# Kernel optimization log

Measured on AMD Instinct MI355X. Metric: run time of the kernel, lower is better.

## Reference

```python
import jax, jax.numpy as jnp
import numpy as np
import math

OUT = 7   # output_size
SR = 2    # sampling_ratio


def _roi_align(feat, rois5, scale):
    """torchvision roi_align (aligned=False) for all rois against one FPN level.
    feat: [B,C,H,W], rois5: [N,5] = (batch_idx, x1, y1, x2, y2). Returns [N,C,OUT,OUT]."""
    B, C, H, W = feat.shape
    b = rois5[:, 0].astype(jnp.int32)
    x1 = rois5[:, 1] * scale
    y1 = rois5[:, 2] * scale
    x2 = rois5[:, 3] * scale
    y2 = rois5[:, 4] * scale
    rw = jnp.maximum(x2 - x1, 1.0)
    rh = jnp.maximum(y2 - y1, 1.0)
    gh = OUT * SR  # sampling grid: ph*SR+iy, sample at (g+0.5)*bin/SR from roi start
    gw = OUT * SR
    ys = y1[:, None] + (jnp.arange(gh, dtype=feat.dtype) + 0.5)[None, :] * (rh / gh)[:, None]  # [N,gh]
    xs = x1[:, None] + (jnp.arange(gw, dtype=feat.dtype) + 0.5)[None, :] * (rw / gw)[:, None]  # [N,gw]
    # torchvision bilinear_interpolate: out-of-range (< -1 or > size) -> 0, else clamp
    vy = (ys >= -1.0) & (ys <= H)
    vx = (xs >= -1.0) & (xs <= W)
    y = jnp.clip(ys, 0.0, H - 1)
    x = jnp.clip(xs, 0.0, W - 1)
    y0f = jnp.floor(y)
    x0f = jnp.floor(x)
    y0 = y0f.astype(jnp.int32)
    x0 = x0f.astype(jnp.int32)
    y1i = jnp.minimum(y0 + 1, H - 1)
    x1i = jnp.minimum(x0 + 1, W - 1)
    ly = y - y0f; hy = 1.0 - ly
    lx = x - x0f; hx = 1.0 - lx
    fT = jnp.transpose(feat, (0, 2, 3, 1))  # [B,H,W,C]

    def gather(yi, xi):
        return fT[b[:, None, None], yi[:, :, None], xi[:, None, :]]  # [N,gh,gw,C]

    w00 = (hy[:, :, None] * hx[:, None, :])[..., None]
    w01 = (hy[:, :, None] * lx[:, None, :])[..., None]
    w10 = (ly[:, :, None] * hx[:, None, :])[..., None]
    w11 = (ly[:, :, None] * lx[:, None, :])[..., None]
    val = (gather(y0, x0) * w00 + gather(y0, x1i) * w01
           + gather(y1i, x0) * w10 + gather(y1i, x1i) * w11)
    val = val * (vy[:, :, None] & vx[:, None, :])[..., None].astype(feat.dtype)
    # average SRxSR samples per output bin -> [N,OUT,OUT,C] -> [N,C,OUT,OUT]
    val = val.reshape(val.shape[0], OUT, SR, OUT, SR, C).mean(axis=(2, 4))
    return jnp.transpose(val, (0, 3, 1, 2))


def setup_inputs() -> dict:
    key = jax.random.key(0)
    ks = jax.random.split(key, 6)
    feat0 = jax.random.normal(ks[0], (2, 256, 200, 200), jnp.float32)
    feat1 = jax.random.normal(ks[1], (2, 256, 100, 100), jnp.float32)
    feat2 = jax.random.normal(ks[2], (2, 256, 50, 50), jnp.float32)
    feat3 = jax.random.normal(ks[3], (2, 256, 25, 25), jnp.float32)
    B, N = 2, 512
    xy1 = jax.random.uniform(ks[4], (B, N, 2), jnp.float32, 0.0, 700.0)
    wh = jax.random.uniform(ks[5], (B, N, 2), jnp.float32, 16.0, 320.0)
    xy2 = jnp.minimum(xy1 + wh, 799.0)
    rois = jnp.concatenate([xy1, xy2], axis=-1)  # [B,N,4] = (x1,y1,x2,y2)
    return {"feat0": feat0, "feat1": feat1, "feat2": feat2, "feat3": feat3,
            "rois": rois, "image_h": 800, "image_w": 800}


def reference(feat0, feat1, feat2, feat3, rois, image_h, image_w):
    feats = [feat0, feat1, feat2, feat3]
    B, N = rois.shape[:2]
    # _convert_to_roi_format: prepend batch index column
    bcol = jnp.repeat(jnp.arange(B, dtype=rois.dtype), N)[:, None]
    rois5 = jnp.concatenate([bcol, rois.reshape(-1, 4)], axis=1)  # [B*N,5]
    # _setup_scales / _get_scales: pow-2-rounded ratio of feature H to image H (static)
    scales = [2.0 ** round(math.log2(f.shape[2] / float(image_h))) for f in feats]
    lvl_min = -math.log2(scales[0])   # 2
    lvl_max = -math.log2(scales[-1])  # 5
    # FPN level routing: k = floor(4 + log2(sqrt(area)/224)), clamped
    area = (rois5[:, 4] - rois5[:, 2]) * (rois5[:, 3] - rois5[:, 1])
    k = jnp.floor(4.0 + jnp.log2(jnp.sqrt(area) / 224.0))
    k = jnp.clip(k, lvl_min, lvl_max) - lvl_min  # in {0,1,2,3}
    out = jnp.zeros((B * N, feats[0].shape[1], OUT, OUT), feats[0].dtype)
    for lvl, (f, s) in enumerate(zip(feats, scales)):
        pooled = _roi_align(f, rois5, s)
        out = jnp.where((k == lvl)[:, None, None, None], pooled, out)
    return out
```

## Files before the change

kernel.cpp:

```cpp
#include <hip/hip_runtime.h>

#define OUTS 7
#define SR 2
#define GRIDW 14
#define NS 196
#define NCH 256
#define NROI 1024
#define NBIN 49

#define L0_OFF 0
#define L1_OFF 20480000
#define L2_OFF 25600000
#define L3_OFF 26880000
#define WS_ELEMS 27200000


static __device__ __forceinline__ unsigned short f2bf(float f) {
    unsigned u = __builtin_bit_cast(unsigned, f);
    u += 0x7fffu + ((u >> 16) & 1u);
    return (unsigned short)(u >> 16);
}

__global__ __launch_bounds__(256) void nchw_to_nhwc_bf16(
    const float* __restrict__ f0, const float* __restrict__ f1,
    const float* __restrict__ f2, const float* __restrict__ f3,
    unsigned short* __restrict__ ws) {
    __shared__ float tile[64][65];
    int bid = blockIdx.x;
    const float* in; unsigned short* outp; int P, ptiles, local;
    if (bid < 5000)      { in = f0; outp = ws + L0_OFF; P = 40000; ptiles = 625; local = bid; }
    else if (bid < 6256) { in = f1; outp = ws + L1_OFF; P = 10000; ptiles = 157; local = bid - 5000; }
    else if (bid < 6576) { in = f2; outp = ws + L2_OFF; P = 2500;  ptiles = 40;  local = bid - 6256; }
    else                 { in = f3; outp = ws + L3_OFF; P = 625;   ptiles = 10;  local = bid - 6576; }
    int pt = local % ptiles;
    int rest = local / ptiles;
    int c0 = (rest & 3) * 64;
    int b  = rest >> 2;
    int p0 = pt * 64;
    int tx = threadIdx.x;
    int ty = threadIdx.y;
    const float* inb = in + (size_t)b * NCH * P;
    unsigned short* outb = outp + (size_t)b * P * NCH;

    int p = p0 + tx;
    if (p < P) {
#pragma unroll
        for (int i = 0; i < 16; ++i) {
            int cl = ty * 16 + i;
            tile[cl][tx] = inb[(size_t)(c0 + cl) * P + p];
        }
    }
    __syncthreads();
#pragma unroll
    for (int i = 0; i < 8; ++i) {
        int pl = ty * 16 + i * 2 + (tx >> 5);
        int cl = (tx & 31) * 2;
        int pp = p0 + pl;
        if (pp < P) {
            unsigned lo = f2bf(tile[cl][pl]);
            unsigned hi = f2bf(tile[cl + 1][pl]);
            *(unsigned*)(outb + (size_t)pp * NCH + c0 + cl) = lo | (hi << 16);
        }
    }
}

__global__ __launch_bounds__(256) void roi_gather_nhwc(
    const unsigned short* __restrict__ nhwc,
    const float* __restrict__ rois,
    float* __restrict__ out) {
    __shared__ int   s_off[4][NS];
    __shared__ float s_w[4][NS];
    __shared__ float lds_out[25 * 260];

    int n = blockIdx.x;
    int tid = threadIdx.x;
    int b = n >> 9;

    float x1 = rois[n * 4 + 0];
    float y1 = rois[n * 4 + 1];
    float x2 = rois[n * 4 + 2];
    float y2 = rois[n * 4 + 3];
    float area = (y2 - y1) * (x2 - x1);
    float kf = floorf(4.0f + log2f(sqrtf(area) / 224.0f));
    kf = fminf(fmaxf(kf, 2.0f), 5.0f);
    int lvl = (int)kf - 2;
    float scale = ldexpf(0.25f, -lvl);
    int H, W; size_t base;
    switch (lvl) {
        case 0:  H = 200; W = 200; base = L0_OFF; break;
        case 1:  H = 100; W = 100; base = L1_OFF; break;
        case 2:  H = 50;  W = 50;  base = L2_OFF; break;
        default: H = 25;  W = 25;  base = L3_OFF; break;
    }
    float x1s = x1 * scale, y1s = y1 * scale;
    float rw = fmaxf(x2 * scale - x1s, 1.0f);
    float rh = fmaxf(y2 * scale - y1s, 1.0f);
    float sx = rw * (1.0f / GRIDW);
    float sy = rh * (1.0f / GRIDW);

    if (tid < NS) {
        int gy = tid / GRIDW, gx = tid % GRIDW;
        float y = y1s + ((float)gy + 0.5f) * sy;
        float x = x1s + ((float)gx + 0.5f) * sx;
        bool valid = (y >= -1.0f) && (y <= (float)H) && (x >= -1.0f) && (x <= (float)W);
        float yc = fminf(fmaxf(y, 0.0f), (float)(H - 1));
        float xc = fminf(fmaxf(x, 0.0f), (float)(W - 1));
        int y0 = (int)floorf(yc), x0 = (int)floorf(xc);
        int y1i = min(y0 + 1, H - 1), x1i = min(x0 + 1, W - 1);
        float ly = yc - (float)y0, lx = xc - (float)x0;
        float hy = 1.0f - ly, hx = 1.0f - lx;
        float vm = valid ? 1.0f : 0.0f;
        s_off[0][tid] = (y0 * W + x0) * NCH;
        s_off[1][tid] = (y0 * W + x1i) * NCH;
        s_off[2][tid] = (y1i * W + x0) * NCH;
        s_off[3][tid] = (y1i * W + x1i) * NCH;
        s_w[0][tid] = hy * hx * vm;
        s_w[1][tid] = hy * lx * vm;
        s_w[2][tid] = ly * hx * vm;
        s_w[3][tid] = ly * lx * vm;
    }
    __syncthreads();

    int lane = tid & 63;
    int wave = tid >> 6;
    const unsigned short* fc = nhwc + base + (size_t)b * (size_t)H * W * NCH + lane * 4;
    float* og = out + (size_t)n * (NCH * NBIN);

#pragma unroll 2
    for (int pass = 0; pass < 2; ++pass) {
        const int b0 = pass * 24;
        const int ncol = pass ? 25 : 24;
        for (int bin = b0 + wave; bin < b0 + ncol; bin += 4) {
            int ph = bin / OUTS, pw = bin % OUTS;
            float4 acc = make_float4(0.f, 0.f, 0.f, 0.f);
#pragma unroll
            for (int iy = 0; iy < SR; ++iy) {
#pragma unroll
                for (int ix = 0; ix < SR; ++ix) {
                    int s = (ph * SR + iy) * GRIDW + (pw * SR + ix);
#pragma unroll
                    for (int t = 0; t < 4; ++t) {
                        float w = s_w[t][s];
                        uint2 v = *(const uint2*)(fc + s_off[t][s]);
                        float a0 = __builtin_bit_cast(float, v.x << 16);
                        float a1 = __builtin_bit_cast(float, v.x & 0xffff0000u);
                        float a2 = __builtin_bit_cast(float, v.y << 16);
                        float a3 = __builtin_bit_cast(float, v.y & 0xffff0000u);
                        acc.x += w * a0;
                        acc.y += w * a1;
                        acc.z += w * a2;
                        acc.w += w * a3;
                    }
                }
            }
            acc.x *= 0.25f; acc.y *= 0.25f; acc.z *= 0.25f; acc.w *= 0.25f;
            *(float4*)&lds_out[(bin - b0) * 260 + lane * 4] = acc;
        }
        __syncthreads();
        for (int i = tid; i < NCH * ncol; i += 256) {
            int c = i / ncol, col = i - c * ncol;
            og[c * NBIN + b0 + col] = lds_out[col * 260 + c];
        }
        __syncthreads();
    }
}


struct RoiMeta {
    float x1, y1, sx, sy;
    int level, b, pad0, pad1;
};

__global__ void prep_rois_kernel(const float* __restrict__ rois,
                                 RoiMeta* __restrict__ meta, int total) {
    int n = blockIdx.x * blockDim.x + threadIdx.x;
    if (n >= total) return;
    float x1 = rois[n * 4 + 0];
    float y1 = rois[n * 4 + 1];
    float x2 = rois[n * 4 + 2];
    float y2 = rois[n * 4 + 3];
    float area = (y2 - y1) * (x2 - x1);
    float k = floorf(4.0f + log2f(sqrtf(area) / 224.0f));
    k = fminf(fmaxf(k, 2.0f), 5.0f);
    int lvl = (int)k - 2;
    float scale = ldexpf(0.25f, -lvl);
    float x1s = x1 * scale;
    float y1s = y1 * scale;
    float rw = fmaxf(x2 * scale - x1s, 1.0f);
    float rh = fmaxf(y2 * scale - y1s, 1.0f);
    RoiMeta m;
    m.x1 = x1s; m.y1 = y1s;
    m.sx = rw / (float)(OUTS * SR);
    m.sy = rh / (float)(OUTS * SR);
    m.level = lvl;
    m.b = n / 512;
    m.pad0 = 0; m.pad1 = 0;
    meta[n] = m;
}

__global__ __launch_bounds__(256) void roi_align_kernel(
    const float* __restrict__ f0, const float* __restrict__ f1,
    const float* __restrict__ f2, const float* __restrict__ f3,
    const RoiMeta* __restrict__ meta, float* __restrict__ out, int total) {
    int idx = blockIdx.x * 256 + threadIdx.x;
    if (idx >= total) return;
    int pw = idx % OUTS;
    int ph = (idx / OUTS) % OUTS;
    int c  = (idx / (OUTS * OUTS)) & (NCH - 1);
    int n  = idx / (OUTS * OUTS * NCH);

    RoiMeta m = meta[n];
    const float* f; int H, W;
    switch (m.level) {
        case 0:  f = f0; H = 200; W = 200; break;
        case 1:  f = f1; H = 100; W = 100; break;
        case 2:  f = f2; H = 50;  W = 50;  break;
        default: f = f3; H = 25;  W = 25;  break;
    }
    const float* fc = f + (size_t)(m.b * NCH + c) * H * W;

    float acc = 0.0f;
#pragma unroll
    for (int iy = 0; iy < SR; ++iy) {
        float y = m.y1 + ((float)(ph * SR + iy) + 0.5f) * m.sy;
        if (y < -1.0f || y > (float)H) continue;
        float yc = fminf(fmaxf(y, 0.0f), (float)(H - 1));
        int y0 = (int)floorf(yc);
        int y1i = min(y0 + 1, H - 1);
        float ly = yc - (float)y0;
        float hy = 1.0f - ly;
        const float* r0 = fc + (size_t)y0 * W;
        const float* r1 = fc + (size_t)y1i * W;
#pragma unroll
        for (int ix = 0; ix < SR; ++ix) {
            float x = m.x1 + ((float)(pw * SR + ix) + 0.5f) * m.sx;
            if (x < -1.0f || x > (float)W) continue;
            float xc = fminf(fmaxf(x, 0.0f), (float)(W - 1));
            int x0 = (int)floorf(xc);
            int x1i = min(x0 + 1, W - 1);
            float lx = xc - (float)x0;
            float hx = 1.0f - lx;
            acc += hy * (hx * r0[x0] + lx * r0[x1i]) +
                   ly * (hx * r1[x0] + lx * r1[x1i]);
        }
    }
    out[idx] = acc * 0.25f;
}


extern "C" void kernel_launch(void* const* d_in, const int* in_sizes, int n_in,
                              void* d_out, int out_size, void* d_ws, size_t ws_size,
                              hipStream_t stream) {
    const float* f0 = (const float*)d_in[0];
    const float* f1 = (const float*)d_in[1];
    const float* f2 = (const float*)d_in[2];
    const float* f3 = (const float*)d_in[3];
    const float* rois = (const float*)d_in[4];
    float* out = (float*)d_out;

    if (ws_size >= (size_t)WS_ELEMS * sizeof(unsigned short)) {
        unsigned short* nhwc = (unsigned short*)d_ws;
        nchw_to_nhwc_bf16<<<6656, dim3(64, 4, 1), 0, stream>>>(f0, f1, f2, f3, nhwc);
        roi_gather_nhwc<<<NROI, 256, 0, stream>>>(nhwc, rois, out);
    } else {
        RoiMeta* meta = (RoiMeta*)d_ws;
        prep_rois_kernel<<<(NROI + 255) / 256, 256, 0, stream>>>(rois, meta, NROI);
        const int total = NROI * NCH * OUTS * OUTS;
        roi_align_kernel<<<(total + 255) / 256, 256, 0, stream>>>(
            f0, f1, f2, f3, meta, out, total);
    }
}
```

Before: 72.59 us.

## Vectorize NCHW-to-NHWC transpose with swizzled LDS and split ROI bins across blocks

The transpose kernel now reads float4 along the spatial axis into an XOR-swizzled shared tile, then writes 8-byte packed bf16 groups of four channels, in place of scalar loads and 4-byte stores. The gather kernel splits each ROI across four blocks of 13 bins, giving four times as many blocks and a smaller shared buffer. The aim is to reduce memory transactions in the transpose, which is bandwidth bound, and to raise occupancy and parallelism in the gather. The trade-off is that each ROI block recomputes the sample offsets and weights, and the output writes for one ROI are spread over four blocks.

Result: slower. 83.01 us (+14.4%).

```diff
diff --git a/kernel.cpp b/kernel.cpp
--- a/kernel.cpp
+++ b/kernel.cpp
@@ -14,7 +14,6 @@
 #define L3_OFF 26880000
 #define WS_ELEMS 27200000
 
-
 static __device__ __forceinline__ unsigned short f2bf(float f) {
     unsigned u = __builtin_bit_cast(unsigned, f);
     u += 0x7fffu + ((u >> 16) & 1u);
@@ -25,7 +24,7 @@
     const float* __restrict__ f0, const float* __restrict__ f1,
     const float* __restrict__ f2, const float* __restrict__ f3,
     unsigned short* __restrict__ ws) {
-    __shared__ float tile[64][65];
+    __shared__ float tile[64 * 66];
     int bid = blockIdx.x;
     const float* in; unsigned short* outp; int P, ptiles, local;
     if (bid < 5000)      { in = f0; outp = ws + L0_OFF; P = 40000; ptiles = 625; local = bid; }
@@ -37,29 +36,59 @@
     int c0 = (rest & 3) * 64;
     int b  = rest >> 2;
     int p0 = pt * 64;
-    int tx = threadIdx.x;
-    int ty = threadIdx.y;
-    const float* inb = in + (size_t)b * NCH * P;
+    int t = threadIdx.x;
+    int l = t & 63, w = t >> 6;
+
+    const float* inb = in + (size_t)(b * NCH + c0) * P;
     unsigned short* outb = outp + (size_t)b * P * NCH;
 
-    int p = p0 + tx;
-    if (p < P) {
-#pragma unroll
-        for (int i = 0; i < 16; ++i) {
-            int cl = ty * 16 + i;
-            tile[cl][tx] = inb[(size_t)(c0 + cl) * P + p];
+    {
+        int px = (l & 15) * 4;
+        int p = p0 + px;
+        if ((P & 3) == 0) {
+#pragma unroll
+            for (int i = 0; i < 4; ++i) {
+                int c = w * 16 + i * 4 + (l >> 4);
+                if (p < P) {
+                    float4 v = *(const float4*)(inb + (size_t)c * P + p);
+                    int pxs = px ^ (((c >> 2) & 7) << 2);
+                    *(float2*)&tile[c * 66 + pxs]     = make_float2(v.x, v.y);
+                    *(float2*)&tile[c * 66 + pxs + 2] = make_float2(v.z, v.w);
+                }
+            }
+        } else {
+#pragma unroll
+            for (int i = 0; i < 4; ++i) {
+                int c = w * 16 + i * 4 + (l >> 4);
+                int pxs = px ^ (((c >> 2) & 7) << 2);
+                const float* src = inb + (size_t)c * P;
+#pragma unroll
+                for (int k = 0; k < 4; ++k) {
+                    tile[c * 66 + pxs + k] = (p + k < P) ? src[p + k] : 0.0f;
+                }
+            }
         }
     }
     __syncthreads();
-#pragma unroll
-    for (int i = 0; i < 8; ++i) {
-        int pl = ty * 16 + i * 2 + (tx >> 5);
-        int cl = (tx & 31) * 2;
-        int pp = p0 + pl;
-        if (pp < P) {
-            unsigned lo = f2bf(tile[cl][pl]);
-            unsigned hi = f2bf(tile[cl + 1][pl]);
-            *(unsigned*)(outb + (size_t)pp * NCH + c0 + cl) = lo | (hi << 16);
+
+    {
+        int j = t & 15;
+        int pb = t >> 4;
+        int S = (j & 7) << 2;
+#pragma unroll
+        for (int it = 0; it < 4; ++it) {
+            int pp = pb + it * 16;
+            int p = p0 + pp;
+            if (p < P) {
+                int pxs = pp ^ S;
+                float a0 = tile[(4 * j + 0) * 66 + pxs];
+                float a1 = tile[(4 * j + 1) * 66 + pxs];
+                float a2 = tile[(4 * j + 2) * 66 + pxs];
+                float a3 = tile[(4 * j + 3) * 66 + pxs];
+                unsigned u0 = (unsigned)f2bf(a0) | ((unsigned)f2bf(a1) << 16);
+                unsigned u1 = (unsigned)f2bf(a2) | ((unsigned)f2bf(a3) << 16);
+                *(uint2*)(outb + (size_t)p * NCH + c0 + 4 * j) = make_uint2(u0, u1);
+            }
         }
     }
 }
@@ -70,9 +99,13 @@
     float* __restrict__ out) {
     __shared__ int   s_off[4][NS];
     __shared__ float s_w[4][NS];
-    __shared__ float lds_out[25 * 260];
-
-    int n = blockIdx.x;
+    __shared__ float lds_out[13 * 260];
+
+    int n = blockIdx.x >> 2;
+    int q = blockIdx.x & 3;
+    int B0 = q * 13;
+    int Bend = min(B0 + 13, NBIN);
+    int ncol = Bend - B0;
     int tid = threadIdx.x;
     int b = n >> 9;
 
@@ -124,44 +157,36 @@
     int lane = tid & 63;
     int wave = tid >> 6;
     const unsigned short* fc = nhwc + base + (size_t)b * (size_t)H * W * NCH + lane * 4;
+
+    for (int bin = B0 + wave; bin < Bend; bin += 4) {
+        int ph = bin / OUTS, pw = bin % OUTS;
+        float4 acc = make_float4(0.f, 0.f, 0.f, 0.f);
+#pragma unroll
+        for (int iy = 0; iy < SR; ++iy) {
+#pragma unroll
+            for (int ix = 0; ix < SR; ++ix) {
+                int s = (ph * SR + iy) * GRIDW + (pw * SR + ix);
+#pragma unroll
+                for (int tp = 0; tp < 4; ++tp) {
+                    float wgt = s_w[tp][s];
+                    uint2 v = *(const uint2*)(fc + s_off[tp][s]);
+                    acc.x += wgt * __builtin_bit_cast(float, v.x << 16);
+                    acc.y += wgt * __builtin_bit_cast(float, v.x & 0xffff0000u);
+                    acc.z += wgt * __builtin_bit_cast(float, v.y << 16);
+                    acc.w += wgt * __builtin_bit_cast(float, v.y & 0xffff0000u);
+                }
+            }
+        }
+        acc.x *= 0.25f; acc.y *= 0.25f; acc.z *= 0.25f; acc.w *= 0.25f;
+        *(float4*)&lds_out[(bin - B0) * 260 + lane * 4] = acc;
+    }
+    __syncthreads();
+
     float* og = out + (size_t)n * (NCH * NBIN);
-
-#pragma unroll 2
-    for (int pass = 0; pass < 2; ++pass) {
-        const int b0 = pass * 24;
-        const int ncol = pass ? 25 : 24;
-        for (int bin = b0 + wave; bin < b0 + ncol; bin += 4) {
-            int ph = bin / OUTS, pw = bin % OUTS;
-            float4 acc = make_float4(0.f, 0.f, 0.f, 0.f);
-#pragma unroll
-            for (int iy = 0; iy < SR; ++iy) {
-#pragma unroll
-                for (int ix = 0; ix < SR; ++ix) {
-                    int s = (ph * SR + iy) * GRIDW + (pw * SR + ix);
-#pragma unroll
-                    for (int t = 0; t < 4; ++t) {
-                        float w = s_w[t][s];
-                        uint2 v = *(const uint2*)(fc + s_off[t][s]);
-                        float a0 = __builtin_bit_cast(float, v.x << 16);
-                        float a1 = __builtin_bit_cast(float, v.x & 0xffff0000u);
-                        float a2 = __builtin_bit_cast(float, v.y << 16);
-                        float a3 = __builtin_bit_cast(float, v.y & 0xffff0000u);
-                        acc.x += w * a0;
-                        acc.y += w * a1;
-                        acc.z += w * a2;
-                        acc.w += w * a3;
-                    }
-                }
-            }
-            acc.x *= 0.25f; acc.y *= 0.25f; acc.z *= 0.25f; acc.w *= 0.25f;
-            *(float4*)&lds_out[(bin - b0) * 260 + lane * 4] = acc;
-        }
-        __syncthreads();
-        for (int i = tid; i < NCH * ncol; i += 256) {
-            int c = i / ncol, col = i - c * ncol;
-            og[c * NBIN + b0 + col] = lds_out[col * 260 + c];
-        }
-        __syncthreads();
+    for (int i = tid; i < 256 * 13; i += 256) {
+        int c = (i * 20165) >> 18;
+        int col = i - c * 13;
+        if (col < ncol) og[c * NBIN + B0 + col] = lds_out[col * 260 + c];
     }
 }
 
@@ -260,8 +285,8 @@
 
     if (ws_size >= (size_t)WS_ELEMS * sizeof(unsigned short)) {
         unsigned short* nhwc = (unsigned short*)d_ws;
-        nchw_to_nhwc_bf16<<<6656, dim3(64, 4, 1), 0, stream>>>(f0, f1, f2, f3, nhwc);
-        roi_gather_nhwc<<<NROI, 256, 0, stream>>>(nhwc, rois, out);
+        nchw_to_nhwc_bf16<<<6656, 256, 0, stream>>>(f0, f1, f2, f3, nhwc);
+        roi_gather_nhwc<<<NROI * 4, 256, 0, stream>>>(nhwc, rois, out);
     } else {
         RoiMeta* meta = (RoiMeta*)d_ws;
         prep_rois_kernel<<<(NROI + 255) / 256, 256, 0, stream>>>(rois, meta, NROI);
```
